# Performance work log

Measured on AMD Instinct MI355X. Metric: run time of the kernel, lower is better.

The kernel has to match this reference:

```python
import jax, jax.numpy as jnp
from jax import lax
import numpy as np

EPS = 1e-5
NEG_SLOPE = 0.2

# 4D conv via lax.conv_general_dilated (supports arbitrary spatial rank)
_DN = ('NCABXY', 'OIABXY', 'NCABXY')  # N,C + 4 spatial dims

def conv4d(x, w):
    # x: (N, Cin, S1, S2, H, W); w: (Cout, Cin, 3, 3, 3, 3); padding=1, stride=1
    return lax.conv_general_dilated(
        x, w,
        window_strides=(1, 1, 1, 1),
        padding=[(1, 1)] * 4,
        dimension_numbers=_DN,
    )

def instance_norm4d(x):
    # normalize per (n, c) over all 4 spatial dims; no affine (PyTorch default)
    mean = jnp.mean(x, axis=(2, 3, 4, 5), keepdims=True)
    var = jnp.var(x, axis=(2, 3, 4, 5), keepdims=True)
    return (x - mean) * lax.rsqrt(var + EPS)

def leaky_relu(x):
    return jnp.where(x >= 0, x, NEG_SLOPE * x)

def setup_inputs() -> dict:
    key = jax.random.key(0)
    k0, k1, k2 = jax.random.split(key, 3)
    image = jax.random.normal(k0, (1, 16, 8, 16, 64, 64), dtype=jnp.float32)
    # He-ish init scale for kernel 3^4
    w1 = jax.random.normal(k1, (32, 16, 3, 3, 3, 3), dtype=jnp.float32) * 0.03
    w2 = jax.random.normal(k2, (32, 32, 3, 3, 3, 3), dtype=jnp.float32) * 0.02
    return {"image": image, "w1": w1, "w2": w2}

def reference(image, w1, w2):
    x = leaky_relu(instance_norm4d(conv4d(image, w1)))
    x = leaky_relu(instance_norm4d(conv4d(x, w2)))
    return x
```

## Files before the change

kernel.cpp:

```cpp
#include <hip/hip_runtime.h>

#define D1 8
#define D2 16
#define HH 64
#define WW 64
#define SPATIAL (D1*D2*HH*WW)
#define EPS 1e-5f
#define NEG 0.2f

typedef unsigned short u16;
typedef __attribute__((ext_vector_type(8))) short s16x8;
typedef __attribute__((ext_vector_type(8))) unsigned short u16x8;
typedef __attribute__((ext_vector_type(4))) unsigned short u16x4;
typedef __attribute__((ext_vector_type(4))) float f32x4;

__device__ __forceinline__ u16 f2bf(float f) {
    unsigned int u = __builtin_bit_cast(unsigned int, f);
    return (u16)((u + 0x7FFFu + ((u >> 16) & 1u)) >> 16);
}
__device__ __forceinline__ float bf2f(u16 u) {
    unsigned int v = ((unsigned int)u) << 16;
    return __builtin_bit_cast(float, v);
}
__device__ __forceinline__ float leaky(float x) {
    return x >= 0.f ? x : NEG * x;
}

__device__ __forceinline__ void decode_block(int flat, int& a, int& b, int& h0) {
    int xcd  = flat & 7;
    int slot = flat >> 3;
    int ht   = slot & 15;
    int b0   = (slot >> 4) & 1;
    a        = (slot >> 5) & 7;
    b        = xcd * 2 + b0;
    h0       = ht * 4;
}

__global__ __launch_bounds__(256)
void prep(const float* __restrict__ img, const float* __restrict__ w1,
          const float* __restrict__ w2, u16* __restrict__ imgT,
          u16* __restrict__ w1t, u16* __restrict__ w2t, float* __restrict__ st)
{
    const int bid = blockIdx.x;
    const int tid = threadIdx.x;
    if (bid < 2048) {
        int p = bid * 256 + tid;
        u16 r[16];
        #pragma unroll
        for (int c = 0; c < 16; ++c)
            r[c] = f2bf(img[(size_t)c * SPATIAL + p]);
        u16x8 lo, hi;
        #pragma unroll
        for (int j = 0; j < 8; ++j) { lo[j] = r[j]; hi[j] = r[8 + j]; }
        u16x8* dst = (u16x8*)(imgT + (size_t)p * 16);
        dst[0] = lo;
        dst[1] = hi;
    } else if (bid < 2264) {
        int i = (bid - 2048) * 256 + tid;
        if (i >= 55296) return;
        int k    = i & 31;
        int co   = (i >> 5) & 31;
        int grp  = (i >> 10) & 1;
        int rest = i >> 11;
        int dh   = rest % 3;
        int p    = rest / 3;
        int da = p / 3, db = p % 3;
        float v = 0.f;
        if (grp == 0) {
            int dw = k >> 4, ci = k & 15;
            v = w1[((((co * 16 + ci) * 3 + da) * 3 + db) * 3 + dh) * 3 + dw];
        } else if (k < 16) {
            v = w1[((((co * 16 + k) * 3 + da) * 3 + db) * 3 + dh) * 3 + 2];
        }
        w1t[i] = f2bf(v);
    } else if (bid < 2588) {
        int i = (bid - 2264) * 256 + tid;
        if (i >= 82944) return;
        int ci = i & 31;
        int co = (i >> 5) & 31;
        int t  = (i >> 10) % 9;
        int p  = (i >> 10) / 9;
        int da = p / 3, db = p % 3, dh = t / 3, dw = t % 3;
        w2t[i] = f2bf(w2[((((co * 32 + ci) * 3 + da) * 3 + db) * 3 + dh) * 3 + dw]);
    } else {
        if (tid < 128) st[tid] = 0.f;
    }
}

#define C1_LDBF(DST, BASE, GRP) { \
    _Pragma("unroll") \
    for (int dh_ = 0; dh_ < 3; ++dh_) { \
        const u16* wb_ = (BASE) + (dh_ * 2 + (GRP)) * 1024; \
        DST[dh_][0] = *(const s16x8*)(wb_ + m * 32 + kq * 8); \
        DST[dh_][1] = *(const s16x8*)(wb_ + (m + 16) * 32 + kq * 8); \
    } }

#define C1_MFMA(BF, CSHIFT) { \
    const int eb_ = (kq & 1) * 8; \
    _Pragma("unroll") \
    for (int x_ = 0; x_ < 6; ++x_) { \
        int pos_ = x_ * 66 + wseg + m + (CSHIFT); \
        s16x8 af_ = *(const s16x8*)&lds[pos_ * 24 + eb_]; \
        _Pragma("unroll") \
        for (int dh_ = 0; dh_ < 3; ++dh_) { \
            int i_ = x_ - dh_; \
            if (i_ >= 0 && i_ < 4) { \
                acc[i_][0] = __builtin_amdgcn_mfma_f32_16x16x32_bf16(af_, BF[dh_][0], acc[i_][0], 0, 0, 0); \
                acc[i_][1] = __builtin_amdgcn_mfma_f32_16x16x32_bf16(af_, BF[dh_][1], acc[i_][1], 0, 0, 0); \
            } \
        } \
    } }

#define C1_PF(K0, K1) { \
    _Pragma("unroll") \
    for (int k_ = (K0); k_ < (K1); ++k_) \
        if ((vmask >> k_) & 1) pf[k_] = *(const u16x8*)(srcn + gbase + k_ * 2048); }

__global__ __launch_bounds__(256, 4)
void conv1_mfma(const u16* __restrict__ xT, const u16* __restrict__ w1t,
                u16* __restrict__ y1, float* __restrict__ st1)
{
    __shared__ __align__(16) u16 lds[396 * 24];
    __shared__ float sred[64];

    const int tid = threadIdx.x;
    int a, b, h0;
    decode_block(blockIdx.x, a, b, h0);
    const int lane = tid & 63;
    const int wv   = tid >> 6;
    const int kq   = lane >> 4;
    const int m    = lane & 15;
    const int wseg = wv << 4;

    unsigned pm = 0;
    #pragma unroll
    for (int p = 0; p < 9; ++p) {
        int ap = a + p / 3 - 1, bp = b + p % 3 - 1;
        if (ap >= 0 && ap < D1 && bp >= 0 && bp < D2) pm |= 1u << p;
    }

    const int p0f  = tid >> 1, g = tid & 1;
    const int hi   = p0f >> 6;
    const int p0c  = p0f & 63;
    unsigned vmask = 0;
    #pragma unroll
    for (int k = 0; k < 3; ++k) {
        int h = h0 - 1 + 2 * k + hi;
        if (h >= 0 && h < HH) vmask |= 1u << k;
    }
    const int gbase = ((h0 - 1 + hi) * WW + p0c) * 16 + g * 8;
    const int lbase = (hi * 66 + p0c + 1) * 24 + g * 8;

    for (int e = tid; e < 396; e += 256) {
        int row = e / 66, col = e - row * 66;
        int h = h0 - 1 + row;
        if (col == 0 || col == 65 || h < 0 || h >= HH) {
            u16x8 z = (u16x8)0;
            *(u16x8*)&lds[e * 24]     = z;
            *(u16x8*)&lds[e * 24 + 8] = z;
        }
    }

    f32x4 acc[4][2];
    #pragma unroll
    for (int i = 0; i < 4; ++i)
        #pragma unroll
        for (int nt = 0; nt < 2; ++nt)
            acc[i][nt] = (f32x4)0.f;

    int p = 0;
    while (!((pm >> p) & 1)) ++p;

    s16x8 bfX[3][2], bfY[3][2];
    C1_LDBF(bfX, w1t + p * 6144, 0);

    u16x8 pf[3];
    {
        const u16* srcn = xT + (size_t)((a + p / 3 - 1) * D2 + (b + p % 3 - 1))
                             * (HH * WW * 16);
        C1_PF(0, 3);
    }

    while (p < 9) {
        int pn = p + 1;
        while (pn < 9 && !((pm >> pn) & 1)) ++pn;

        #pragma unroll
        for (int k = 0; k < 3; ++k)
            if ((vmask >> k) & 1) *(u16x8*)&lds[lbase + k * 3168] = pf[k];
        __syncthreads();

        const u16* srcn = nullptr;
        if (pn < 9)
            srcn = xT + (size_t)((a + pn / 3 - 1) * D2 + (b + pn % 3 - 1))
                      * (HH * WW * 16);

        const u16* wbase = w1t + p * 6144;

        C1_LDBF(bfY, wbase, 1);
        C1_MFMA(bfX, (kq >> 1));
        if (pn < 9) C1_PF(0, 2);

        C1_MFMA(bfY, 2);
        if (pn < 9) C1_PF(2, 3);

        __syncthreads();
        if (pn < 9) C1_LDBF(bfX, w1t + pn * 6144, 0);
        p = pn;
    }

    if (tid < 64) sred[tid] = 0.f;
    __syncthreads();

    float s[2] = {0.f, 0.f}, s2[2] = {0.f, 0.f};
    const size_t plane_out = (size_t)(a * D2 + b) * (HH * WW);
    #pragma unroll
    for (int i = 0; i < 4; ++i) {
        int h  = h0 + i;
        int w0 = wseg + kq * 4;
        #pragma unroll
        for (int nt = 0; nt < 2; ++nt) {
            int co = m + nt * 16;
            #pragma unroll
            for (int reg = 0; reg < 4; ++reg) {
                float v = acc[i][nt][reg];
                s[nt]  += v;
                s2[nt] += v * v;
                y1[(plane_out + h * WW + (w0 + reg)) * 32 + co] = f2bf(v);
            }
        }
    }
    #pragma unroll
    for (int nt = 0; nt < 2; ++nt) {
        s[nt]  += __shfl_xor(s[nt], 16);  s[nt]  += __shfl_xor(s[nt], 32);
        s2[nt] += __shfl_xor(s2[nt], 16); s2[nt] += __shfl_xor(s2[nt], 32);
    }
    if (kq == 0) {
        atomicAdd(&sred[m * 2],            s[0]);
        atomicAdd(&sred[m * 2 + 1],        s2[0]);
        atomicAdd(&sred[(m + 16) * 2],     s[1]);
        atomicAdd(&sred[(m + 16) * 2 + 1], s2[1]);
    }
    __syncthreads();
    if (tid < 64) atomicAdd(&st1[tid], sred[tid]);
}

__global__ __launch_bounds__(256)
void norm1_kernel(u16* __restrict__ y1, const float* __restrict__ st1)
{
    const int tid = threadIdx.x;
    const int q   = tid & 3;
    const float invN = 1.f / (float)SPATIAL;
    float mean[8], scl[8];
    #pragma unroll
    for (int j = 0; j < 8; ++j) {
        int ci  = q * 8 + j;
        float mu = st1[ci * 2] * invN;
        float va = st1[ci * 2 + 1] * invN - mu * mu;
        mean[j] = mu;
        scl[j]  = rsqrtf(va + EPS);
    }
    #pragma unroll
    for (int j4 = 0; j4 < 4; ++j4) {
        size_t gidx = (size_t)blockIdx.x * 1024 + j4 * 256 + tid;
        u16x8* ptr = (u16x8*)(y1 + gidx * 8);
        u16x8 v = *ptr;
        u16x8 o;
        #pragma unroll
        for (int j = 0; j < 8; ++j)
            o[j] = f2bf(leaky((bf2f(v[j]) - mean[j]) * scl[j]));
        *ptr = o;
    }
}

#define C2_LDBF(DST, BASE, DW) { \
    _Pragma("unroll") \
    for (int dh_ = 0; dh_ < 3; ++dh_) { \
        const u16* wb_ = (BASE) + (dh_ * 3 + (DW)) * 1024; \
        DST[dh_][0] = *(const s16x8*)(wb_ + m * 32 + kq * 8); \
        DST[dh_][1] = *(const s16x8*)(wb_ + (m + 16) * 32 + kq * 8); \
    } }

#define C2_MFMA(BF, DW) { \
    _Pragma("unroll") \
    for (int x_ = 0; x_ < 6; ++x_) { \
        int pos_ = x_ * 66 + wseg + (DW) + m; \
        s16x8 af_ = *(const s16x8*)&lds[pos_ * 40 + kq * 8]; \
        _Pragma("unroll") \
        for (int dh_ = 0; dh_ < 3; ++dh_) { \
            int i_ = x_ - dh_; \
            if (i_ >= 0 && i_ < 4) { \
                acc[i_][0] = __builtin_amdgcn_mfma_f32_16x16x32_bf16(af_, BF[dh_][0], acc[i_][0], 0, 0, 0); \
                acc[i_][1] = __builtin_amdgcn_mfma_f32_16x16x32_bf16(af_, BF[dh_][1], acc[i_][1], 0, 0, 0); \
            } \
        } \
    } }

#define C2_PF(K0, K1) { \
    _Pragma("unroll") \
    for (int k_ = (K0); k_ < (K1); ++k_) \
        if ((vmask >> k_) & 1) pf[k_] = *(const u16x8*)(srcn + gbase + k_ * 2048); }

__global__ __launch_bounds__(256, 3)
void conv2_mfma(const u16* __restrict__ y1, const u16* __restrict__ w2t,
                u16* __restrict__ y2, float* __restrict__ st2)
{
    __shared__ __align__(16) u16 lds[396 * 40];
    __shared__ float sred[64];

    const int tid = threadIdx.x;
    int a, b, h0;
    decode_block(blockIdx.x, a, b, h0);
    const int lane = tid & 63;
    const int wv   = tid >> 6;
    const int kq   = lane >> 4;
    const int m    = lane & 15;
    const int wseg = wv << 4;

    unsigned pm = 0;
    #pragma unroll
    for (int p = 0; p < 9; ++p) {
        int ap = a + p / 3 - 1, bp = b + p % 3 - 1;
        if (ap >= 0 && ap < D1 && bp >= 0 && bp < D2) pm |= 1u << p;
    }

    const int p0 = tid >> 2, q = tid & 3;
    unsigned vmask = 0;
    #pragma unroll
    for (int k = 0; k < 6; ++k) {
        int h = h0 - 1 + k;
        if (h >= 0 && h < HH) vmask |= 1u << k;
    }
    const int gbase = ((h0 - 1) * WW + p0) * 32 + q * 8;
    const int lbase = (p0 + 1) * 40 + q * 8;

    for (int e = tid; e < 396; e += 256) {
        int row = e / 66, col = e - row * 66;
        int h = h0 - 1 + row;
        if (col == 0 || col == 65 || h < 0 || h >= HH) {
            u16x8 z = (u16x8)0;
            #pragma unroll
            for (int gg = 0; gg < 4; ++gg)
                *(u16x8*)&lds[e * 40 + gg * 8] = z;
        }
    }

    f32x4 acc[4][2];
    #pragma unroll
    for (int i = 0; i < 4; ++i)
        #pragma unroll
        for (int nt = 0; nt < 2; ++nt)
            acc[i][nt] = (f32x4)0.f;

    int p = 0;
    while (!((pm >> p) & 1)) ++p;

    s16x8 bfX[3][2], bfY[3][2];
    C2_LDBF(bfX, w2t + p * 9216, 0);

    u16x8 pf[6];
    {
        const u16* srcn = y1 + (size_t)((a + p / 3 - 1) * D2 + (b + p % 3 - 1))
                             * (HH * WW * 32);
        C2_PF(0, 6);
    }

    while (p < 9) {
        int pn = p + 1;
        while (pn < 9 && !((pm >> pn) & 1)) ++pn;

        #pragma unroll
        for (int k = 0; k < 6; ++k)
            if ((vmask >> k) & 1) *(u16x8*)&lds[lbase + k * 2640] = pf[k];
        __syncthreads();

        const u16* srcn = nullptr;
        if (pn < 9)
            srcn = y1 + (size_t)((a + pn / 3 - 1) * D2 + (b + pn % 3 - 1))
                      * (HH * WW * 32);

        const u16* wbase = w2t + p * 9216;

        C2_LDBF(bfY, wbase, 1);
        C2_MFMA(bfX, 0);
        if (pn < 9) C2_PF(0, 2);

        C2_LDBF(bfX, wbase, 2);
        C2_MFMA(bfY, 1);
        if (pn < 9) C2_PF(2, 4);

        C2_MFMA(bfX, 2);
        if (pn < 9) C2_PF(4, 6);

        __syncthreads();
        if (pn < 9) C2_LDBF(bfX, w2t + pn * 9216, 0);
        p = pn;
    }

    if (tid < 64) sred[tid] = 0.f;
    __syncthreads();

    float s[2] = {0.f, 0.f}, s2[2] = {0.f, 0.f};
    #pragma unroll
    for (int i = 0; i < 4; ++i) {
        int h  = h0 + i;
        int w0 = wseg + kq * 4;
        #pragma unroll
        for (int nt = 0; nt < 2; ++nt) {
            int co = m + nt * 16;
            u16x4 pk;
            #pragma unroll
            for (int reg = 0; reg < 4; ++reg) {
                float v = acc[i][nt][reg];
                s[nt]  += v;
                s2[nt] += v * v;
                pk[reg] = f2bf(v);
            }
            size_t off = ((size_t)(co * D1 + a) * D2 + b) * (HH * WW) + h * WW + w0;
            *(u16x4*)(y2 + off) = pk;
        }
    }
    #pragma unroll
    for (int nt = 0; nt < 2; ++nt) {
        s[nt]  += __shfl_xor(s[nt], 16);  s[nt]  += __shfl_xor(s[nt], 32);
        s2[nt] += __shfl_xor(s2[nt], 16); s2[nt] += __shfl_xor(s2[nt], 32);
    }
    if (kq == 0) {
        atomicAdd(&sred[m * 2],            s[0]);
        atomicAdd(&sred[m * 2 + 1],        s2[0]);
        atomicAdd(&sred[(m + 16) * 2],     s[1]);
        atomicAdd(&sred[(m + 16) * 2 + 1], s2[1]);
    }
    __syncthreads();
    if (tid < 64) atomicAdd(&st2[tid], sred[tid]);
}

__global__ __launch_bounds__(256)
void norm2_kernel(const u16* __restrict__ y2, const float* __restrict__ st2,
                  float* __restrict__ out)
{
    size_t i8 = (size_t)blockIdx.x * 256 + threadIdx.x;
    int c = (int)(i8 >> 16);
    const float invN = 1.f / (float)SPATIAL;
    float mu = st2[c * 2] * invN;
    float va = st2[c * 2 + 1] * invN - mu * mu;
    float sc = rsqrtf(va + EPS);
    u16x8 v = *(const u16x8*)(y2 + i8 * 8);
    float4 o0, o1;
    o0.x = leaky((bf2f(v[0]) - mu) * sc);
    o0.y = leaky((bf2f(v[1]) - mu) * sc);
    o0.z = leaky((bf2f(v[2]) - mu) * sc);
    o0.w = leaky((bf2f(v[3]) - mu) * sc);
    o1.x = leaky((bf2f(v[4]) - mu) * sc);
    o1.y = leaky((bf2f(v[5]) - mu) * sc);
    o1.z = leaky((bf2f(v[6]) - mu) * sc);
    o1.w = leaky((bf2f(v[7]) - mu) * sc);
    float4* dst = (float4*)(out + i8 * 8);
    dst[0] = o0;
    dst[1] = o1;
}

extern "C" void kernel_launch(void* const* d_in, const int* in_sizes, int n_in,
                              void* d_out, int out_size, void* d_ws, size_t ws_size,
                              hipStream_t stream)
{
    const float* image = (const float*)d_in[0];
    const float* w1    = (const float*)d_in[1];
    const float* w2    = (const float*)d_in[2];
    float* out = (float*)d_out;

    u16*   imgT = (u16*)d_ws;
    u16*   y1   = (u16*)((char*)d_ws + 33554432);
    u16*   y2   = imgT;
    float* st   = (float*)((char*)d_ws + 67108864);
    float* st1  = st;
    float* st2  = st + 64;

    u16* w1t = (u16*)((char*)d_out + 66832384);
    u16* w2t = (u16*)((char*)d_out + 66942976);

    prep<<<2589, 256, 0, stream>>>(image, w1, w2, imgT, w1t, w2t, st);

    conv1_mfma<<<2048, 256, 0, stream>>>(imgT, w1t, y1, st1);
    norm1_kernel<<<2048, 256, 0, stream>>>(y1, st1);
    conv2_mfma<<<2048, 256, 0, stream>>>(y1, w2t, y2, st2);
    norm2_kernel<<<8192, 256, 0, stream>>>(y2, st2, out);
}
```

Baseline: 291.1 us.

## Double conv block height to 8 rows with 512-thread blocks

Each conv block now computes 8 output rows instead of 4, using 8 waves, so the LDS tile holds 10 input rows instead of 6. This cuts the redundant halo loads per output row, from 1.5x to 1.25x, and halves the grid size. The cost is more LDS per block and larger blocks, which may lower occupancy or scheduling flexibility, and the load mapping and vmask logic had to be rewritten.

```diff
diff --git a/kernel.cpp b/kernel.cpp
--- a/kernel.cpp
+++ b/kernel.cpp
@@ -29,11 +29,11 @@
 __device__ __forceinline__ void decode_block(int flat, int& a, int& b, int& h0) {
     int xcd  = flat & 7;
     int slot = flat >> 3;
-    int ht   = slot & 15;
-    int b0   = (slot >> 4) & 1;
-    a        = (slot >> 5) & 7;
+    int ht   = slot & 7;
+    int b0   = (slot >> 3) & 1;
+    a        = (slot >> 4) & 7;
     b        = xcd * 2 + b0;
-    h0       = ht * 4;
+    h0       = ht * 8;
 }
 
 __global__ __launch_bounds__(256)
@@ -99,14 +99,14 @@
     const int eb_ = (kq & 1) * 8; \
     _Pragma("unroll") \
     for (int x_ = 0; x_ < 6; ++x_) { \
-        int pos_ = x_ * 66 + wseg + m + (CSHIFT); \
+        int pos_ = (i0 + x_) * 66 + wseg + m + (CSHIFT); \
         s16x8 af_ = *(const s16x8*)&lds[pos_ * 24 + eb_]; \
         _Pragma("unroll") \
         for (int dh_ = 0; dh_ < 3; ++dh_) { \
-            int i_ = x_ - dh_; \
-            if (i_ >= 0 && i_ < 4) { \
-                acc[i_][0] = __builtin_amdgcn_mfma_f32_16x16x32_bf16(af_, BF[dh_][0], acc[i_][0], 0, 0, 0); \
-                acc[i_][1] = __builtin_amdgcn_mfma_f32_16x16x32_bf16(af_, BF[dh_][1], acc[i_][1], 0, 0, 0); \
+            int li_ = x_ - dh_; \
+            if (li_ >= 0 && li_ < 4) { \
+                acc[li_][0] = __builtin_amdgcn_mfma_f32_16x16x32_bf16(af_, BF[dh_][0], acc[li_][0], 0, 0, 0); \
+                acc[li_][1] = __builtin_amdgcn_mfma_f32_16x16x32_bf16(af_, BF[dh_][1], acc[li_][1], 0, 0, 0); \
             } \
         } \
     } }
@@ -114,13 +114,13 @@
 #define C1_PF(K0, K1) { \
     _Pragma("unroll") \
     for (int k_ = (K0); k_ < (K1); ++k_) \
-        if ((vmask >> k_) & 1) pf[k_] = *(const u16x8*)(srcn + gbase + k_ * 2048); }
-
-__global__ __launch_bounds__(256, 4)
+        if ((vmask >> k_) & 1) pf[k_] = *(const u16x8*)(srcn + gbase + k_ * 4096); }
+
+__global__ __launch_bounds__(512, 4)
 void conv1_mfma(const u16* __restrict__ xT, const u16* __restrict__ w1t,
                 u16* __restrict__ y1, float* __restrict__ st1)
 {
-    __shared__ __align__(16) u16 lds[396 * 24];
+    __shared__ __align__(16) u16 lds[660 * 24];
     __shared__ float sred[64];
 
     const int tid = threadIdx.x;
@@ -130,7 +130,8 @@
     const int wv   = tid >> 6;
     const int kq   = lane >> 4;
     const int m    = lane & 15;
-    const int wseg = wv << 4;
+    const int wseg = (wv & 3) << 4;
+    const int i0   = (wv >> 2) * 4;
 
     unsigned pm = 0;
     #pragma unroll
@@ -139,22 +140,22 @@
         if (ap >= 0 && ap < D1 && bp >= 0 && bp < D2) pm |= 1u << p;
     }
 
-    const int p0f  = tid >> 1, g = tid & 1;
-    const int hi   = p0f >> 6;
-    const int p0c  = p0f & 63;
+    const int g = tid & 1, cr = tid >> 1;
+    const int col = cr & 63, rq = cr >> 6;
     unsigned vmask = 0;
     #pragma unroll
     for (int k = 0; k < 3; ++k) {
-        int h = h0 - 1 + 2 * k + hi;
-        if (h >= 0 && h < HH) vmask |= 1u << k;
-    }
-    const int gbase = ((h0 - 1 + hi) * WW + p0c) * 16 + g * 8;
-    const int lbase = (hi * 66 + p0c + 1) * 24 + g * 8;
-
-    for (int e = tid; e < 396; e += 256) {
-        int row = e / 66, col = e - row * 66;
+        int row = rq + 4 * k;
         int h = h0 - 1 + row;
-        if (col == 0 || col == 65 || h < 0 || h >= HH) {
+        if (row < 10 && h >= 0 && h < HH) vmask |= 1u << k;
+    }
+    const int gbase = ((h0 - 1 + rq) * WW + col) * 16 + g * 8;
+    const int lbase = (rq * 66 + col + 1) * 24 + g * 8;
+
+    for (int e = tid; e < 660; e += 512) {
+        int row = e / 66, c2 = e - row * 66;
+        int h = h0 - 1 + row;
+        if (c2 == 0 || c2 == 65 || h < 0 || h >= HH) {
             u16x8 z = (u16x8)0;
             *(u16x8*)&lds[e * 24]     = z;
             *(u16x8*)&lds[e * 24 + 8] = z;
@@ -187,7 +188,7 @@
 
         #pragma unroll
         for (int k = 0; k < 3; ++k)
-            if ((vmask >> k) & 1) *(u16x8*)&lds[lbase + k * 3168] = pf[k];
+            if ((vmask >> k) & 1) *(u16x8*)&lds[lbase + k * 6336] = pf[k];
         __syncthreads();
 
         const u16* srcn = nullptr;
@@ -216,7 +217,7 @@
     const size_t plane_out = (size_t)(a * D2 + b) * (HH * WW);
     #pragma unroll
     for (int i = 0; i < 4; ++i) {
-        int h  = h0 + i;
+        int h  = h0 + i0 + i;
         int w0 = wseg + kq * 4;
         #pragma unroll
         for (int nt = 0; nt < 2; ++nt) {
@@ -284,14 +285,14 @@
 #define C2_MFMA(BF, DW) { \
     _Pragma("unroll") \
     for (int x_ = 0; x_ < 6; ++x_) { \
-        int pos_ = x_ * 66 + wseg + (DW) + m; \
+        int pos_ = (i0 + x_) * 66 + wseg + (DW) + m; \
         s16x8 af_ = *(const s16x8*)&lds[pos_ * 40 + kq * 8]; \
         _Pragma("unroll") \
         for (int dh_ = 0; dh_ < 3; ++dh_) { \
-            int i_ = x_ - dh_; \
-            if (i_ >= 0 && i_ < 4) { \
-                acc[i_][0] = __builtin_amdgcn_mfma_f32_16x16x32_bf16(af_, BF[dh_][0], acc[i_][0], 0, 0, 0); \
-                acc[i_][1] = __builtin_amdgcn_mfma_f32_16x16x32_bf16(af_, BF[dh_][1], acc[i_][1], 0, 0, 0); \
+            int li_ = x_ - dh_; \
+            if (li_ >= 0 && li_ < 4) { \
+                acc[li_][0] = __builtin_amdgcn_mfma_f32_16x16x32_bf16(af_, BF[dh_][0], acc[li_][0], 0, 0, 0); \
+                acc[li_][1] = __builtin_amdgcn_mfma_f32_16x16x32_bf16(af_, BF[dh_][1], acc[li_][1], 0, 0, 0); \
             } \
         } \
     } }
@@ -299,13 +300,13 @@
 #define C2_PF(K0, K1) { \
     _Pragma("unroll") \
     for (int k_ = (K0); k_ < (K1); ++k_) \
-        if ((vmask >> k_) & 1) pf[k_] = *(const u16x8*)(srcn + gbase + k_ * 2048); }
-
-__global__ __launch_bounds__(256, 3)
+        if ((vmask >> k_) & 1) pf[k_] = *(const u16x8*)(srcn + gbase + k_ * 4096); }
+
+__global__ __launch_bounds__(512, 4)
 void conv2_mfma(const u16* __restrict__ y1, const u16* __restrict__ w2t,
                 u16* __restrict__ y2, float* __restrict__ st2)
 {
-    __shared__ __align__(16) u16 lds[396 * 40];
+    __shared__ __align__(16) u16 lds[660 * 40];
     __shared__ float sred[64];
 
     const int tid = threadIdx.x;
@@ -315,7 +316,8 @@
     const int wv   = tid >> 6;
     const int kq   = lane >> 4;
     const int m    = lane & 15;
-    const int wseg = wv << 4;
+    const int wseg = (wv & 3) << 4;
+    const int i0   = (wv >> 2) * 4;
 
     unsigned pm = 0;
     #pragma unroll
@@ -324,20 +326,21 @@
         if (ap >= 0 && ap < D1 && bp >= 0 && bp < D2) pm |= 1u << p;
     }
 
-    const int p0 = tid >> 2, q = tid & 3;
+    const int q = tid & 3, cr = tid >> 2;
+    const int col = cr & 63, rh = cr >> 6;
     unsigned vmask = 0;
     #pragma unroll
-    for (int k = 0; k < 6; ++k) {
-        int h = h0 - 1 + k;
+    for (int k = 0; k < 5; ++k) {
+        int h = h0 - 1 + rh + 2 * k;
         if (h >= 0 && h < HH) vmask |= 1u << k;
     }
-    const int gbase = ((h0 - 1) * WW + p0) * 32 + q * 8;
-    const int lbase = (p0 + 1) * 40 + q * 8;
-
-    for (int e = tid; e < 396; e += 256) {
-        int row = e / 66, col = e - row * 66;
+    const int gbase = ((h0 - 1 + rh) * WW + col) * 32 + q * 8;
+    const int lbase = (rh * 66 + col + 1) * 40 + q * 8;
+
+    for (int e = tid; e < 660; e += 512) {
+        int row = e / 66, c2 = e - row * 66;
         int h = h0 - 1 + row;
-        if (col == 0 || col == 65 || h < 0 || h >= HH) {
+        if (c2 == 0 || c2 == 65 || h < 0 || h >= HH) {
             u16x8 z = (u16x8)0;
             #pragma unroll
             for (int gg = 0; gg < 4; ++gg)
@@ -358,11 +361,11 @@
     s16x8 bfX[3][2], bfY[3][2];
     C2_LDBF(bfX, w2t + p * 9216, 0);
 
-    u16x8 pf[6];
+    u16x8 pf[5];
     {
         const u16* srcn = y1 + (size_t)((a + p / 3 - 1) * D2 + (b + p % 3 - 1))
                              * (HH * WW * 32);
-        C2_PF(0, 6);
+        C2_PF(0, 5);
     }
 
     while (p < 9) {
@@ -370,8 +373,8 @@
         while (pn < 9 && !((pm >> pn) & 1)) ++pn;
 
         #pragma unroll
-        for (int k = 0; k < 6; ++k)
-            if ((vmask >> k) & 1) *(u16x8*)&lds[lbase + k * 2640] = pf[k];
+        for (int k = 0; k < 5; ++k)
+            if ((vmask >> k) & 1) *(u16x8*)&lds[lbase + k * 5280] = pf[k];
         __syncthreads();
 
         const u16* srcn = nullptr;
@@ -390,7 +393,7 @@
         if (pn < 9) C2_PF(2, 4);
 
         C2_MFMA(bfX, 2);
-        if (pn < 9) C2_PF(4, 6);
+        if (pn < 9) C2_PF(4, 5);
 
         __syncthreads();
         if (pn < 9) C2_LDBF(bfX, w2t + pn * 9216, 0);
@@ -403,7 +406,7 @@
     float s[2] = {0.f, 0.f}, s2[2] = {0.f, 0.f};
     #pragma unroll
     for (int i = 0; i < 4; ++i) {
-        int h  = h0 + i;
+        int h  = h0 + i0 + i;
         int w0 = wseg + kq * 4;
         #pragma unroll
         for (int nt = 0; nt < 2; ++nt) {
@@ -481,8 +484,8 @@
 
     prep<<<2589, 256, 0, stream>>>(image, w1, w2, imgT, w1t, w2t, st);
 
-    conv1_mfma<<<2048, 256, 0, stream>>>(imgT, w1t, y1, st1);
+    conv1_mfma<<<1024, 512, 0, stream>>>(imgT, w1t, y1, st1);
     norm1_kernel<<<2048, 256, 0, stream>>>(y1, st1);
-    conv2_mfma<<<2048, 256, 0, stream>>>(y1, w2t, y2, st2);
+    conv2_mfma<<<1024, 512, 0, stream>>>(y1, w2t, y2, st2);
     norm2_kernel<<<8192, 256, 0, stream>>>(y2, st2, out);
 }
```

Result: faster. 281.5 us (-3.3%).
